# Kernel optimization log

Measured on AMD Instinct MI355X. Metric: run time of the kernel, lower is better.

## Reference

```python
import jax, jax.numpy as jnp
import numpy as np

H = 32          # hidden_dim (forced by targetLayer = Linear(4*32, 1))
IN = 1          # input_size per step
T = 129         # seq_len
S = 4           # 4 parallel LSTM streams: [main, f1, f2, f3]


def setup_inputs() -> dict:
    key = jax.random.key(0)
    ks = jax.random.split(key, 16)
    sc = 1.0 / np.sqrt(H)
    u = lambda k, shape: jax.random.uniform(k, shape, jnp.float32, -sc, sc)
    inp = {
        "x": jax.random.normal(ks[0], (S, T, IN), jnp.float32),
        # layer 0 (input -> hidden), stacked over the 4 LSTMs; gate order i,f,g,o
        "Wih0": u(ks[1], (S, 4 * H, IN)),
        "Whh0": u(ks[2], (S, 4 * H, H)),
        "bih0": u(ks[3], (S, 4 * H)),
        "bhh0": u(ks[4], (S, 4 * H)),
        # layer 1 (hidden -> hidden)
        "Wih1": u(ks[5], (S, 4 * H, H)),
        "Whh1": u(ks[6], (S, 4 * H, H)),
        "bih1": u(ks[7], (S, 4 * H)),
        "bhh1": u(ks[8], (S, 4 * H)),
        # output heads
        "Wt": u(ks[9], (1, 4 * H)),
        "bt": u(ks[10], (1,)),
        "Wf1": u(ks[11], (1, H)),
        "bf1": u(ks[12], (1,)),
        "Wf2": u(ks[13], (1, H)),
        "bf2": u(ks[14], (1,)),
    }
    return inp


def _cell(xin, h, c, Wih, Whh, bih, bhh):
    # xin: [S, in], h/c: [S, H]; fused 4-stream LSTM cell, PyTorch gate order i,f,g,o
    g = jnp.einsum('sgi,si->sg', Wih, xin) + jnp.einsum('sgh,sh->sg', Whh, h) + bih + bhh
    i, f, gg, o = jnp.split(g, 4, axis=-1)
    c2 = jax.nn.sigmoid(f) * c + jax.nn.sigmoid(i) * jnp.tanh(gg)
    h2 = jax.nn.sigmoid(o) * jnp.tanh(c2)
    return h2, c2


def reference(x, Wih0, Whh0, bih0, bhh0, Wih1, Whh1, bih1, bhh1, Wt, bt, Wf1, bf1, Wf2, bf2):
    z = jnp.zeros((S, H), x.dtype)

    def step(carry, xt):
        h0, c0, h1, c1 = carry
        h0, c0 = _cell(xt, h0, c0, Wih0, Whh0, bih0, bhh0)
        h1, c1 = _cell(h0, h1, c1, Wih1, Whh1, bih1, bhh1)
        return (h0, c0, h1, c1), None

    xs = jnp.transpose(x, (1, 0, 2))  # [T, S, IN]
    (h0, c0, h1, c1), _ = jax.lax.scan(step, (z, z, z, z), xs)
    hlast = h1  # [S, H], last-step top-layer output; order: main, f1, f2, f3

    targetIn = hlast.reshape(1, S * H)          # torch.cat(...).view(-1, 4H)
    targetOut = targetIn @ Wt.T + bt            # [1, 1]
    f1Out = (hlast[1:2] @ Wf1.T + bf1).reshape(1, 1, 1)
    f2Out = (hlast[2:3] @ Wf2.T + bf2).reshape(1, 1, 1)
    f3Out = (hlast[3:4] @ Wf2.T + bf2).reshape(1, 1, 1)  # original bug: reuses featureLayer2
    return (targetOut, f1Out, f2Out, f3Out)
```

## Files before the change

### kernel.cpp

```cpp
#include <hip/hip_runtime.h>


#define HDIM 32
#define SEQT 129
#define NS 4

__device__ __forceinline__ float fsig(float x) {
  return __builtin_amdgcn_rcpf(1.0f + __expf(-x));
}
__device__ __forceinline__ float swap_hi(float v) {
  auto r = __builtin_amdgcn_permlane32_swap(__float_as_int(v), __float_as_int(v),
                                            false, false);
  return __int_as_float(r[1]);
}

__device__ __forceinline__ float dot32(const float* __restrict__ w,
                                       const float* __restrict__ h, float seed) {
  float a0 = seed, a1 = 0.f, a2 = 0.f, a3 = 0.f;
  float a4 = 0.f, a5 = 0.f, a6 = 0.f, a7 = 0.f;
  #pragma unroll
  for (int j = 0; j < 4; ++j) {
    a0 = fmaf(w[8*j+0], h[8*j+0], a0);
    a1 = fmaf(w[8*j+1], h[8*j+1], a1);
    a2 = fmaf(w[8*j+2], h[8*j+2], a2);
    a3 = fmaf(w[8*j+3], h[8*j+3], a3);
    a4 = fmaf(w[8*j+4], h[8*j+4], a4);
    a5 = fmaf(w[8*j+5], h[8*j+5], a5);
    a6 = fmaf(w[8*j+6], h[8*j+6], a6);
    a7 = fmaf(w[8*j+7], h[8*j+7], a7);
  }
  return ((a0 + a1) + (a2 + a3)) + ((a4 + a5) + (a6 + a7));
}

__global__ __launch_bounds__(256)
void lstm4_kernel(const float* __restrict__ x,
                  const float* __restrict__ Wih0, const float* __restrict__ Whh0,
                  const float* __restrict__ bih0, const float* __restrict__ bhh0,
                  const float* __restrict__ Wih1, const float* __restrict__ Whh1,
                  const float* __restrict__ bih1, const float* __restrict__ bhh1,
                  const float* __restrict__ Wt,  const float* __restrict__ bt,
                  const float* __restrict__ Wf1, const float* __restrict__ bf1,
                  const float* __restrict__ Wf2, const float* __restrict__ bf2,
                  float* __restrict__ out) {
  const int tid = threadIdx.x;
  const int s = tid >> 6;
  const int l = tid & 63;

  __shared__ float xs[NS * SEQT + 1];
  __shared__ __align__(16) float hb0[NS][HDIM];
  __shared__ __align__(16) float hb1[NS][HDIM];

  for (int i = tid; i < NS * SEQT; i += 256) xs[i] = x[i];
  if (tid == 0) xs[NS * SEQT] = 0.0f;
  for (int i = tid; i < NS * HDIM; i += 256) {
    (&hb0[0][0])[i] = 0.0f;
    (&hb1[0][0])[i] = 0.0f;
  }
  __syncthreads();

  const int r1 = s * 128 + l;
  const int r2 = s * 128 + l + 64;

  float wh0a[HDIM], wh0b[HDIM], wi1a[HDIM], wi1b[HDIM], wh1a[HDIM], wh1b[HDIM];
  #pragma unroll
  for (int j = 0; j < 8; ++j) {
    float4 v;
    v = *(const float4*)(Whh0 + r1 * 32 + 4 * j);
    wh0a[4*j] = v.x; wh0a[4*j+1] = v.y; wh0a[4*j+2] = v.z; wh0a[4*j+3] = v.w;
    v = *(const float4*)(Whh0 + r2 * 32 + 4 * j);
    wh0b[4*j] = v.x; wh0b[4*j+1] = v.y; wh0b[4*j+2] = v.z; wh0b[4*j+3] = v.w;
    v = *(const float4*)(Wih1 + r1 * 32 + 4 * j);
    wi1a[4*j] = v.x; wi1a[4*j+1] = v.y; wi1a[4*j+2] = v.z; wi1a[4*j+3] = v.w;
    v = *(const float4*)(Wih1 + r2 * 32 + 4 * j);
    wi1b[4*j] = v.x; wi1b[4*j+1] = v.y; wi1b[4*j+2] = v.z; wi1b[4*j+3] = v.w;
    v = *(const float4*)(Whh1 + r1 * 32 + 4 * j);
    wh1a[4*j] = v.x; wh1a[4*j+1] = v.y; wh1a[4*j+2] = v.z; wh1a[4*j+3] = v.w;
    v = *(const float4*)(Whh1 + r2 * 32 + 4 * j);
    wh1b[4*j] = v.x; wh1b[4*j+1] = v.y; wh1b[4*j+2] = v.z; wh1b[4*j+3] = v.w;
  }
  const float wx0a = Wih0[r1];
  const float wx0b = Wih0[r2];
  const float b0a  = bih0[r1] + bhh0[r1];
  const float b0b  = bih0[r2] + bhh0[r2];
  const float b1a  = bih1[r1] + bhh1[r1];
  const float b1b  = bih1[r2] + bhh1[r2];

  const bool  lo   = (l < 32);
  const float m2   = lo ? 2.0f : 1.0f;
  const float add2 = lo ? -1.0f : 0.0f;

  float c0 = 0.0f, c1 = 0.0f;
  float h1new = 0.0f;

  float hv[HDIM];
  #pragma unroll
  for (int k = 0; k < HDIM; ++k) hv[k] = 0.0f;

  float xt = xs[s * SEQT];

  #pragma unroll 1
  for (int t = 0; t < SEQT; ++t) {
    const float xt_next = xs[s * SEQT + t + 1];

    float gv[HDIM];
    #pragma unroll
    for (int j = 0; j < 8; ++j) {
      const float4 g4 = *(const float4*)&hb1[s][4 * j];
      gv[4*j] = g4.x; gv[4*j+1] = g4.y; gv[4*j+2] = g4.z; gv[4*j+3] = g4.w;
    }

    const float v1 = dot32(wh0a, hv, fmaf(wx0a, xt, b0a));
    const float v2 = dot32(wh0b, hv, fmaf(wx0b, xt, b0b));

    const float e1 = dot32(wh1a, gv, b1a);
    const float e2 = dot32(wh1b, gv, b1b);

    const float a1  = fsig(v1);
    const float sv2 = fsig(v2 * m2);
    const float a2  = fmaf(sv2, m2, add2);
    const float p   = a1 * a2;
    const float swf = swap_hi(a1);
    const float swo = swap_hi(a2);
    c0 = fmaf(swf, c0, p);
    const float th0 = fmaf(fsig(2.0f * c0), 2.0f, -1.0f);
    const float h0new = swo * th0;

    if (lo) hb0[s][l] = h0new;

    float hv2[HDIM];
    #pragma unroll
    for (int j = 0; j < 8; ++j) {
      const float4 h4 = *(const float4*)&hb0[s][4 * j];
      hv2[4*j] = h4.x; hv2[4*j+1] = h4.y; hv2[4*j+2] = h4.z; hv2[4*j+3] = h4.w;
    }

    const float w1 = dot32(wi1a, hv2, e1);
    const float w2 = dot32(wi1b, hv2, e2);

    const float A1  = fsig(w1);
    const float sw2 = fsig(w2 * m2);
    const float A2  = fmaf(sw2, m2, add2);
    const float P   = A1 * A2;
    const float SWF = swap_hi(A1);
    const float SWO = swap_hi(A2);
    c1 = fmaf(SWF, c1, P);
    const float th1 = fmaf(fsig(2.0f * c1), 2.0f, -1.0f);
    h1new = SWO * th1;

    if (lo) hb1[s][l] = h1new;

    #pragma unroll
    for (int k = 0; k < HDIM; ++k) hv[k] = hv2[k];

    xt = xt_next;
  }

  __syncthreads();

  float acc = 0.0f;
  if (s == 0) {
    acc = fmaf(Wt[l], (&hb1[0][0])[l], Wt[l + 64] * (&hb1[0][0])[l + 64]);
  } else {
    const float* Wf = (s == 1) ? Wf1 : Wf2;
    if (l < HDIM) acc = Wf[l] * hb1[s][l];
  }
  #pragma unroll
  for (int off = 32; off > 0; off >>= 1) acc += __shfl_xor(acc, off);
  if (l == 0) {
    const float bias = (s == 0) ? bt[0] : ((s == 1) ? bf1[0] : bf2[0]);
    out[s] = acc + bias;
  }
}

extern "C" void kernel_launch(void* const* d_in, const int* in_sizes, int n_in,
                              void* d_out, int out_size, void* d_ws, size_t ws_size,
                              hipStream_t stream) {
  const float* x    = (const float*)d_in[0];
  const float* Wih0 = (const float*)d_in[1];
  const float* Whh0 = (const float*)d_in[2];
  const float* bih0 = (const float*)d_in[3];
  const float* bhh0 = (const float*)d_in[4];
  const float* Wih1 = (const float*)d_in[5];
  const float* Whh1 = (const float*)d_in[6];
  const float* bih1 = (const float*)d_in[7];
  const float* bhh1 = (const float*)d_in[8];
  const float* Wt   = (const float*)d_in[9];
  const float* bt   = (const float*)d_in[10];
  const float* Wf1  = (const float*)d_in[11];
  const float* bf1  = (const float*)d_in[12];
  const float* Wf2  = (const float*)d_in[13];
  const float* bf2  = (const float*)d_in[14];
  float* out = (float*)d_out;

  lstm4_kernel<<<1, 256, 0, stream>>>(x, Wih0, Whh0, bih0, bhh0,
                                      Wih1, Whh1, bih1, bhh1,
                                      Wt, bt, Wf1, bf1, Wf2, bf2, out);
}
```

Baseline: 177.5 us.

## Use packed FMA dot products and compute next-step layer-0 gates early

Recasts the weight registers and hidden-state reads as float2 vectors so the dot products can lower to packed FMA instructions, halving the FMA instruction count. It also restructures the recurrence: the layer-0 gate pre-activations for step t+1 are computed right after h0 for step t is available, in the same block as the layer-1 dot products. This removes one serial phase per timestep and drops the register copy of the hidden vector. Risks are different register pressure and a changed floating-point summation order.

```diff
diff --git a/kernel.cpp b/kernel.cpp
--- a/kernel.cpp
+++ b/kernel.cpp
@@ -4,6 +4,8 @@
 #define HDIM 32
 #define SEQT 129
 #define NS 4
+
+typedef float f32x2 __attribute__((ext_vector_type(2)));
 
 __device__ __forceinline__ float fsig(float x) {
   return __builtin_amdgcn_rcpf(1.0f + __expf(-x));
@@ -14,22 +16,18 @@
   return __int_as_float(r[1]);
 }
 
-__device__ __forceinline__ float dot32(const float* __restrict__ w,
-                                       const float* __restrict__ h, float seed) {
-  float a0 = seed, a1 = 0.f, a2 = 0.f, a3 = 0.f;
-  float a4 = 0.f, a5 = 0.f, a6 = 0.f, a7 = 0.f;
+__device__ __forceinline__ float pkdot(const f32x2* __restrict__ w,
+                                       const f32x2* __restrict__ h, float seed) {
+  f32x2 a0 = {seed, 0.f}, a1 = {0.f, 0.f}, a2 = {0.f, 0.f}, a3 = {0.f, 0.f};
   #pragma unroll
   for (int j = 0; j < 4; ++j) {
-    a0 = fmaf(w[8*j+0], h[8*j+0], a0);
-    a1 = fmaf(w[8*j+1], h[8*j+1], a1);
-    a2 = fmaf(w[8*j+2], h[8*j+2], a2);
-    a3 = fmaf(w[8*j+3], h[8*j+3], a3);
-    a4 = fmaf(w[8*j+4], h[8*j+4], a4);
-    a5 = fmaf(w[8*j+5], h[8*j+5], a5);
-    a6 = fmaf(w[8*j+6], h[8*j+6], a6);
-    a7 = fmaf(w[8*j+7], h[8*j+7], a7);
+    a0 = __builtin_elementwise_fma(w[4*j+0], h[4*j+0], a0);
+    a1 = __builtin_elementwise_fma(w[4*j+1], h[4*j+1], a1);
+    a2 = __builtin_elementwise_fma(w[4*j+2], h[4*j+2], a2);
+    a3 = __builtin_elementwise_fma(w[4*j+3], h[4*j+3], a3);
   }
-  return ((a0 + a1) + (a2 + a3)) + ((a4 + a5) + (a6 + a7));
+  const f32x2 r = (a0 + a1) + (a2 + a3);
+  return r.x + r.y;
 }
 
 __global__ __launch_bounds__(256)
@@ -61,22 +59,15 @@
   const int r1 = s * 128 + l;
   const int r2 = s * 128 + l + 64;
 
-  float wh0a[HDIM], wh0b[HDIM], wi1a[HDIM], wi1b[HDIM], wh1a[HDIM], wh1b[HDIM];
+  f32x2 wh0a[16], wh0b[16], wi1a[16], wi1b[16], wh1a[16], wh1b[16];
   #pragma unroll
-  for (int j = 0; j < 8; ++j) {
-    float4 v;
-    v = *(const float4*)(Whh0 + r1 * 32 + 4 * j);
-    wh0a[4*j] = v.x; wh0a[4*j+1] = v.y; wh0a[4*j+2] = v.z; wh0a[4*j+3] = v.w;
-    v = *(const float4*)(Whh0 + r2 * 32 + 4 * j);
-    wh0b[4*j] = v.x; wh0b[4*j+1] = v.y; wh0b[4*j+2] = v.z; wh0b[4*j+3] = v.w;
-    v = *(const float4*)(Wih1 + r1 * 32 + 4 * j);
-    wi1a[4*j] = v.x; wi1a[4*j+1] = v.y; wi1a[4*j+2] = v.z; wi1a[4*j+3] = v.w;
-    v = *(const float4*)(Wih1 + r2 * 32 + 4 * j);
-    wi1b[4*j] = v.x; wi1b[4*j+1] = v.y; wi1b[4*j+2] = v.z; wi1b[4*j+3] = v.w;
-    v = *(const float4*)(Whh1 + r1 * 32 + 4 * j);
-    wh1a[4*j] = v.x; wh1a[4*j+1] = v.y; wh1a[4*j+2] = v.z; wh1a[4*j+3] = v.w;
-    v = *(const float4*)(Whh1 + r2 * 32 + 4 * j);
-    wh1b[4*j] = v.x; wh1b[4*j+1] = v.y; wh1b[4*j+2] = v.z; wh1b[4*j+3] = v.w;
+  for (int j = 0; j < 16; ++j) {
+    wh0a[j] = *(const f32x2*)(Whh0 + r1 * 32 + 2 * j);
+    wh0b[j] = *(const f32x2*)(Whh0 + r2 * 32 + 2 * j);
+    wi1a[j] = *(const f32x2*)(Wih1 + r1 * 32 + 2 * j);
+    wi1b[j] = *(const f32x2*)(Wih1 + r2 * 32 + 2 * j);
+    wh1a[j] = *(const f32x2*)(Whh1 + r1 * 32 + 2 * j);
+    wh1b[j] = *(const f32x2*)(Whh1 + r2 * 32 + 2 * j);
   }
   const float wx0a = Wih0[r1];
   const float wx0b = Wih0[r2];
@@ -90,30 +81,18 @@
   const float add2 = lo ? -1.0f : 0.0f;
 
   float c0 = 0.0f, c1 = 0.0f;
-  float h1new = 0.0f;
 
-  float hv[HDIM];
-  #pragma unroll
-  for (int k = 0; k < HDIM; ++k) hv[k] = 0.0f;
-
-  float xt = xs[s * SEQT];
+  float xt0 = xs[s * SEQT];
+  float v1 = fmaf(wx0a, xt0, b0a);
+  float v2 = fmaf(wx0b, xt0, b0b);
 
   #pragma unroll 1
   for (int t = 0; t < SEQT; ++t) {
-    const float xt_next = xs[s * SEQT + t + 1];
+    f32x2 gv[16];
+    #pragma unroll
+    for (int j = 0; j < 16; ++j) gv[j] = *(const f32x2*)&hb1[s][2 * j];
 
-    float gv[HDIM];
-    #pragma unroll
-    for (int j = 0; j < 8; ++j) {
-      const float4 g4 = *(const float4*)&hb1[s][4 * j];
-      gv[4*j] = g4.x; gv[4*j+1] = g4.y; gv[4*j+2] = g4.z; gv[4*j+3] = g4.w;
-    }
-
-    const float v1 = dot32(wh0a, hv, fmaf(wx0a, xt, b0a));
-    const float v2 = dot32(wh0b, hv, fmaf(wx0b, xt, b0b));
-
-    const float e1 = dot32(wh1a, gv, b1a);
-    const float e2 = dot32(wh1b, gv, b1b);
+    const float xtn = xs[s * SEQT + t + 1];
 
     const float a1  = fsig(v1);
     const float sv2 = fsig(v2 * m2);
@@ -127,15 +106,18 @@
 
     if (lo) hb0[s][l] = h0new;
 
-    float hv2[HDIM];
+    f32x2 hv[16];
     #pragma unroll
-    for (int j = 0; j < 8; ++j) {
-      const float4 h4 = *(const float4*)&hb0[s][4 * j];
-      hv2[4*j] = h4.x; hv2[4*j+1] = h4.y; hv2[4*j+2] = h4.z; hv2[4*j+3] = h4.w;
-    }
+    for (int j = 0; j < 16; ++j) hv[j] = *(const f32x2*)&hb0[s][2 * j];
 
-    const float w1 = dot32(wi1a, hv2, e1);
-    const float w2 = dot32(wi1b, hv2, e2);
+    const float e1 = pkdot(wh1a, gv, b1a);
+    const float e2 = pkdot(wh1b, gv, b1b);
+
+    const float w1 = pkdot(wi1a, hv, e1);
+    const float w2 = pkdot(wi1b, hv, e2);
+
+    v1 = pkdot(wh0a, hv, fmaf(wx0a, xtn, b0a));
+    v2 = pkdot(wh0b, hv, fmaf(wx0b, xtn, b0b));
 
     const float A1  = fsig(w1);
     const float sw2 = fsig(w2 * m2);
@@ -145,14 +127,9 @@
     const float SWO = swap_hi(A2);
     c1 = fmaf(SWF, c1, P);
     const float th1 = fmaf(fsig(2.0f * c1), 2.0f, -1.0f);
-    h1new = SWO * th1;
+    const float h1new = SWO * th1;
 
     if (lo) hb1[s][l] = h1new;
-
-    #pragma unroll
-    for (int k = 0; k < HDIM; ++k) hv[k] = hv2[k];
-
-    xt = xt_next;
   }
 
   __syncthreads();
```

Result: faster. 154.1 us (-13.2%).
